# Kernel optimization log

Hardware: AMD Instinct MI355X
Metric: run time of the kernel (lower is better)

Reference implementation:

```python
import jax, jax.numpy as jnp
import numpy as np

B = 4096      # number of trees
DEPTH = 7     # complete binary tree depth -> N = 2**DEPTH - 1 = 127 nodes (heap order)
I_DIM = 300
H_DIM = 150


def setup_inputs() -> dict:
    key = jax.random.key(0)
    ks = jax.random.split(key, 6)
    N = 2 ** DEPTH - 1
    x = jax.random.normal(ks[0], (B, N, I_DIM), dtype=jnp.float32)
    Wiuo = jax.random.normal(ks[1], (3 * H_DIM, I_DIM), dtype=jnp.float32) / np.sqrt(I_DIM)
    Uiuo = jax.random.normal(ks[2], (3 * H_DIM, H_DIM), dtype=jnp.float32) / np.sqrt(H_DIM)
    biuo = jax.random.normal(ks[3], (1, 3 * H_DIM), dtype=jnp.float32) * 0.02
    Uf_w = jax.random.normal(ks[4], (H_DIM, H_DIM), dtype=jnp.float32) / np.sqrt(H_DIM)
    Uf_b = jax.random.normal(ks[5], (H_DIM,), dtype=jnp.float32) * 0.02
    return {"x": x, "Wiuo": Wiuo, "Uiuo": Uiuo, "biuo": biuo, "Uf_w": Uf_w, "Uf_b": Uf_b}


def reference(x, Wiuo, Uiuo, biuo, Uf_w, Uf_b):
    # Child-sum Tree-LSTM on complete binary trees (heap ordering).
    # Level d occupies node indices [2^d - 1, 2^(d+1) - 1); leaves at d = DEPTH-1.
    Bsz, N, _ = x.shape
    H = Uf_w.shape[0]
    # Input projection for all nodes (dropout in eval mode = identity)
    iuo_x = jnp.einsum('bni,ki->bnk', x, Wiuo)  # [B, N, 3H]
    h = jnp.zeros((Bsz, N, H), x.dtype)
    c = jnp.zeros((Bsz, N, H), x.dtype)
    for d in reversed(range(DEPTH)):  # leaves -> root (static loop over tree levels)
        start = 2 ** d - 1
        size = 2 ** d
        iuo = iuo_x[:, start:start + size]  # [B, size, 3H]
        if d == DEPTH - 1:
            c_sum = jnp.zeros((Bsz, size, H), x.dtype)
        else:
            cstart = 2 ** (d + 1) - 1
            ch = h[:, cstart:cstart + 2 * size].reshape(Bsz, size, 2, H)
            cc = c[:, cstart:cstart + 2 * size].reshape(Bsz, size, 2, H)
            h_tilda = ch.sum(axis=2)  # sum of children hidden states
            f = jax.nn.sigmoid(jnp.einsum('bskh,gh->bskg', ch, Uf_w) + Uf_b)
            c_sum = (f * cc).sum(axis=2)
            iuo = iuo + jnp.einsum('bsh,kh->bsk', h_tilda, Uiuo)
        iuo = iuo + biuo
        i_g, u_g, o_g = jnp.split(iuo, 3, axis=-1)
        c_new = jax.nn.sigmoid(i_g) * jnp.tanh(u_g) + c_sum
        h_new = jax.nn.sigmoid(o_g) * jnp.tanh(c_new)
        h = h.at[:, start:start + size].set(h_new)
        c = c.at[:, start:start + size].set(c_new)
    return h
```

## Files before the change

kernel.cpp:

```cpp
#include <hip/hip_runtime.h>

typedef float  f32x4  __attribute__((ext_vector_type(4)));
typedef short  s16x8  __attribute__((ext_vector_type(8)));
typedef short  s16x4  __attribute__((ext_vector_type(4)));
typedef _Float16 f16;

namespace {
constexpr int NN = 127, IDIM = 300, HD = 150;
constexpr int NT = 640, NW = 10;
constexpr int BCS  = 36;
constexpr int WSLAB = 17408;
constexpr int WCH = 34;
constexpr int ASTR = 36;
constexpr int A_SH = 64 * ASTR;
constexpr int GEMM_LDS = (2 * A_SH + 2 * WSLAB) * 2;
constexpr int CSTR = 164;

constexpr int W_SH = 10 * WSLAB;
constexpr int U_SH = 480 * 160;
constexpr int F_SH = 160 * 160;

constexpr size_t C_N   = (size_t)4096 * 126 * HD;
constexpr size_t IUO_N = (size_t)4096 * 63 * 456;

__device__ __forceinline__ short f2bf(float f) {
    union { __bf16 b; short s; } u; u.b = (__bf16)f; return u.s;
}
__device__ __forceinline__ float bf2f(short s) {
    union { float f; unsigned u; } v; v.u = ((unsigned)(unsigned short)s) << 16; return v.f;
}
__device__ __forceinline__ float sig_(float x)  { return 1.0f / (1.0f + __expf(-x)); }
__device__ __forceinline__ float tanh_(float x) { float e = __expf(2.0f * x); return 1.0f - 2.0f / (e + 1.0f); }
__device__ __forceinline__ s16x4 cvt4(float a,float b,float c,float d) {
    return s16x4{ f2bf(a), f2bf(b), f2bf(c), f2bf(d) };
}
__device__ __forceinline__ s16x8 cat(s16x4 lo, s16x4 hi) {
    return __builtin_shufflevector(lo, hi, 0,1,2,3,4,5,6,7);
}
__device__ __forceinline__ f32x4 MFMA(s16x8 a, s16x8 b, f32x4 c) {
    return __builtin_amdgcn_mfma_f32_16x16x32_bf16(a, b, c, 0, 0, 0);
}

typedef const __attribute__((address_space(1))) unsigned int* gp_t;
typedef __attribute__((address_space(3))) unsigned int* lp_t;
__device__ __forceinline__ void stage_slab(const short* g, short* l, int nch, int wv, int ln) {
    const char* gb = (const char*)g;
    char* lb = (char*)l;
    for (int c = wv; c < nch; c += NW)
        __builtin_amdgcn_global_load_lds((gp_t)(gb + c * 1024 + ln * 16),
                                         (lp_t)(lb + c * 1024 + ln * 16), 16, 0, 0);
}
}

__global__ __launch_bounds__(256)
void prep_w(const float* __restrict__ Wiuo, const float* __restrict__ Uiuo,
            const float* __restrict__ Ufw, short* __restrict__ dst) {
    int i = blockIdx.x * 256 + threadIdx.x;
    short v = 0;
    if (i < W_SH) {
        int kc = i / WSLAB, r = i - kc * WSLAB;
        if (r < 480 * BCS) {
            int col = r / BCS, j = r - col * BCS;
            int g = col / 160, cp = col - g * 160, k = kc * 32 + j;
            if (cp < HD && j < 32 && k < IDIM) v = f2bf(Wiuo[(size_t)(g*HD + cp)*IDIM + k]);
        }
        dst[i] = v;
    } else if (i < W_SH + U_SH) {
        int q = i - W_SH;
        int col = q / 160, k = q - col * 160;
        int g = col / 160, cp = col - g * 160;
        if (cp < HD && k < HD) v = f2bf(Uiuo[(size_t)(g*HD + cp)*HD + k]);
        dst[i] = v;
    } else if (i < W_SH + U_SH + F_SH) {
        int q = i - W_SH - U_SH;
        int col = q / 160, k = q - col * 160;
        if (col < HD && k < HD) v = f2bf(Ufw[(size_t)col*HD + k]);
        dst[i] = v;
    }
}

__global__ __launch_bounds__(NT)
void big_gemm(const float* __restrict__ x, const short* __restrict__ Wsl,
              const float* __restrict__ biuo, float* __restrict__ h_all,
              f16* __restrict__ c_all, f16* __restrict__ iuo_all)
{
    extern __shared__ short smem[];
    short* A0 = smem;
    short* A1 = A0 + A_SH;
    short* B0 = A1 + A_SH;
    short* B1 = B0 + WSLAB;

    const int t = threadIdx.x;
    const int wv = t >> 6, ln = t & 63, l15 = ln & 15, kg = ln >> 4;
    const int row0 = blockIdx.x * 64;

    int d = 6;
    for (int dd = 0; dd <= 5; ++dd)
        if (row0 >= 4096 * (128 - (2 << dd))) { d = dd; break; }
    const int base = 4096 * (128 - (2 << d));
    const int lg = d, mask = (1 << lg) - 1, start = (1 << lg) - 1;
    const int local0 = row0 - base;

    const int sr = t >> 3, sq = t & 7;
    const float* xrow = nullptr;
    if (sr < 64) {
        int lcl = local0 + sr, b = lcl >> lg, s = lcl & mask;
        xrow = x + ((size_t)b * NN + start + s) * IDIM;
    }

    stage_slab(Wsl, B0, WCH, wv, ln);
    if (sr < 64) {
        float4 f = *(const float4*)(xrow + sq * 4);
        *(s16x4*)&A0[sr * ASTR + sq * 4] = cvt4(f.x, f.y, f.z, f.w);
    }
    __syncthreads();

    f32x4 acc[4][3] = {};
    #pragma unroll
    for (int kc = 0; kc < 10; ++kc) {
        short* Ac = (kc & 1) ? A1 : A0;
        short* An = (kc & 1) ? A0 : A1;
        short* Bc = (kc & 1) ? B1 : B0;
        short* Bn = (kc & 1) ? B0 : B1;
        float4 nxt = {0.f, 0.f, 0.f, 0.f};
        if (kc < 9) {
            stage_slab(Wsl + (kc + 1) * WSLAB, Bn, WCH, wv, ln);
            if (sr < 64) {
                int k0 = (kc + 1) * 32 + sq * 4;
                if (k0 + 3 < IDIM) nxt = *(const float4*)(xrow + k0);
            }
        }
        s16x8 a[4];
        #pragma unroll
        for (int mt = 0; mt < 4; ++mt) {
            const short* p = &Ac[(16*mt + l15) * ASTR + kg * 8];
            a[mt] = cat(*(const s16x4*)p, *(const s16x4*)(p + 4));
        }
        #pragma unroll
        for (int g = 0; g < 3; ++g) {
            const short* p = &Bc[(g*160 + 16*wv + l15) * BCS + kg * 8];
            s16x8 bf = cat(*(const s16x4*)p, *(const s16x4*)(p + 4));
            #pragma unroll
            for (int mt = 0; mt < 4; ++mt)
                acc[mt][g] = MFMA(a[mt], bf, acc[mt][g]);
        }
        if (kc < 9) {
            if (sr < 64)
                *(s16x4*)&An[sr * ASTR + sq * 4] = cvt4(nxt.x, nxt.y, nxt.z, nxt.w);
            __syncthreads();
        }
    }

    const int c = 16 * wv + l15;
    if (c < HD) {
        if (d == 6) {
            float bi = biuo[c], bu = biuo[HD + c], bo = biuo[2*HD + c];
            #pragma unroll
            for (int mt = 0; mt < 4; ++mt)
                #pragma unroll
                for (int r = 0; r < 4; ++r) {
                    int lcl = local0 + 16*mt + 4*kg + r;
                    int b = lcl >> 6, s = lcl & 63;
                    float cn = sig_(acc[mt][0][r] + bi) * tanh_(acc[mt][1][r] + bu);
                    float hn = sig_(acc[mt][2][r] + bo) * tanh_(cn);
                    h_all[((size_t)b*NN + 63 + s) * HD + c] = hn;
                    c_all[((size_t)b*126 + 62 + s) * HD + c] = (f16)cn;
                }
        } else {
            #pragma unroll
            for (int mt = 0; mt < 4; ++mt)
                #pragma unroll
                for (int r = 0; r < 4; ++r) {
                    int lcl = local0 + 16*mt + 4*kg + r;
                    int b = lcl >> lg, s = lcl & mask;
                    f16* ip = iuo_all + ((size_t)b*63 + start + s) * 456;
                    ip[c]       = (f16)acc[mt][0][r];
                    ip[152 + c] = (f16)acc[mt][1][r];
                    ip[304 + c] = (f16)acc[mt][2][r];
                }
        }
    }
}

__global__ __launch_bounds__(NT, 5)
void lvl_light(const short* __restrict__ Ubf, const short* __restrict__ Fbf,
               const float* __restrict__ biuo, const float* __restrict__ Ufb,
               const f16* __restrict__ iuo_all, f16* __restrict__ c_all,
               float* __restrict__ h_all, int start, int lg, int cstart)
{
    __shared__ short chs[2][16][CSTR];
    __shared__ short fgs[NW][32][16];

    const int t = threadIdx.x;
    const int wv = t >> 6, ln = t & 63, l15 = ln & 15, kg = ln >> 4;
    const int row0 = blockIdx.x * 16;
    const int mask = (1 << lg) - 1;
    const int c = wv * 16 + l15;

    {
        int rc = t & 31, part = t >> 5;
        int plane = rc >> 4, lr = rc & 15;
        int row = row0 + lr, b = row >> lg, s = row & mask;
        const float* hp = h_all + ((size_t)b*NN + cstart + 2*s + plane) * HD;
        short* dst = &chs[plane][lr][part * 8];
        if (part < 18) {
            float4 f0 = *(const float4*)(hp + part*8);
            float4 f1 = *(const float4*)(hp + part*8 + 4);
            *(s16x4*)dst       = cvt4(f0.x, f0.y, f0.z, f0.w);
            *(s16x4*)(dst + 4) = cvt4(f1.x, f1.y, f1.z, f1.w);
        } else if (part == 18) {
            float4 f0 = *(const float4*)(hp + 144);
            float2 f1 = *(const float2*)(hp + 148);
            *(s16x4*)dst       = cvt4(f0.x, f0.y, f0.z, f0.w);
            *(s16x4*)(dst + 4) = s16x4{ f2bf(f1.x), f2bf(f1.y), 0, 0 };
        } else {
            *(s16x4*)dst = s16x4{0,0,0,0};
            *(s16x4*)(dst + 4) = s16x4{0,0,0,0};
        }
    }
    __syncthreads();

    f32x4 facc[2] = {};
    #pragma unroll
    for (int kc = 0; kc < 5; ++kc) {
        int ka = kc * 32 + kg * 8;
        s16x8 bf = *(const s16x8*)(Fbf + (size_t)c * 160 + ka);
        #pragma unroll
        for (int rt = 0; rt < 2; ++rt) {
            const short* p = &chs[rt][l15][ka];
            s16x8 af = cat(*(const s16x4*)p, *(const s16x4*)(p + 4));
            facc[rt] = MFMA(af, bf, facc[rt]);
        }
    }
    {
        float fb_ = (c < HD) ? Ufb[c] : 0.0f;
        #pragma unroll
        for (int rt = 0; rt < 2; ++rt)
            #pragma unroll
            for (int r = 0; r < 4; ++r)
                fgs[wv][rt*16 + 4*kg + r][l15] = f2bf(sig_(facc[rt][r] + fb_));
    }
    __syncthreads();

    f32x4 acc[3] = {};
    #pragma unroll
    for (int kc = 0; kc < 5; ++kc) {
        int ka = kc * 32 + kg * 8;
        const short* p0 = &chs[0][l15][ka];
        const short* p1 = &chs[1][l15][ka];
        s16x8 h0 = cat(*(const s16x4*)p0, *(const s16x4*)(p0 + 4));
        s16x8 h1 = cat(*(const s16x4*)p1, *(const s16x4*)(p1 + 4));
        s16x8 hs;
        #pragma unroll
        for (int e = 0; e < 8; ++e)
            hs[e] = f2bf(bf2f(h0[e]) + bf2f(h1[e]));
        #pragma unroll
        for (int g = 0; g < 3; ++g) {
            s16x8 bf = *(const s16x8*)(Ubf + (size_t)(g*160 + c) * 160 + ka);
            acc[g] = MFMA(hs, bf, acc[g]);
        }
    }

    if (c < HD) {
        float bi = biuo[c], bu = biuo[HD + c], bo = biuo[2*HD + c];
        #pragma unroll
        for (int r = 0; r < 4; ++r) {
            int pl = 4*kg + r;
            int row = row0 + pl, b = row >> lg, s = row & mask;
            const f16* ip = iuo_all + ((size_t)b*63 + start + s) * 456;
            float ig = (float)ip[c]       + bi + acc[0][r];
            float ug = (float)ip[152 + c] + bu + acc[1][r];
            float og = (float)ip[304 + c] + bo + acc[2][r];
            float f0 = bf2f(fgs[wv][pl][l15]);
            float f1 = bf2f(fgs[wv][16 + pl][l15]);
            size_t ci = (size_t)b*126 + (cstart + 2*s - 1);
            float c0 = (float)c_all[ci * HD + c];
            float c1 = (float)c_all[(ci + 1) * HD + c];
            float cn = sig_(ig) * tanh_(ug) + f0*c0 + f1*c1;
            float hn = sig_(og) * tanh_(cn);
            h_all[((size_t)b*NN + start + s) * HD + c] = hn;
            if (start > 0)
                c_all[((size_t)b*126 + start + s - 1) * HD + c] = (f16)cn;
        }
    }
}

extern "C" void kernel_launch(void* const* d_in, const int* in_sizes, int n_in,
                              void* d_out, int out_size, void* d_ws, size_t ws_size,
                              hipStream_t stream) {
    const float* x    = (const float*)d_in[0];
    const float* Wiuo = (const float*)d_in[1];
    const float* Uiuo = (const float*)d_in[2];
    const float* biuo = (const float*)d_in[3];
    const float* Ufw  = (const float*)d_in[4];
    const float* Ufb  = (const float*)d_in[5];
    float* h = (float*)d_out;

    f16* c_all   = (f16*)d_ws;
    f16* iuo_all = c_all + C_N;
    short* slabs = (short*)(iuo_all + IUO_N);
    const short* Wsl = slabs;
    const short* Ubf = slabs + W_SH;
    const short* Fbf = slabs + W_SH + U_SH;

    (void)hipFuncSetAttribute((const void*)big_gemm,
                              hipFuncAttributeMaxDynamicSharedMemorySize, 160 * 1024);

    prep_w<<<(W_SH + U_SH + F_SH + 255) / 256, 256, 0, stream>>>(Wiuo, Uiuo, Ufw, slabs);

    big_gemm<<<8128, NT, GEMM_LDS, stream>>>(x, Wsl, biuo, h, c_all, iuo_all);

    for (int d = 5; d >= 0; --d) {
        const int start = (1 << d) - 1, cstart = (1 << (d+1)) - 1;
        lvl_light<<<256 << d, NT, 0, stream>>>(Ubf, Fbf, biuo, Ufb, iuo_all, c_all, h,
                                               start, d, cstart);
    }
}
```

Baseline: 1.076 ms.

## Shrink GEMM tiles, single-buffer weight slab, halve level-kernel threads

```diff
diff --git a/kernel.cpp b/kernel.cpp
--- a/kernel.cpp
+++ b/kernel.cpp
@@ -8,15 +8,16 @@
 namespace {
 constexpr int NN = 127, IDIM = 300, HD = 150;
 constexpr int NT = 640, NW = 10;
-constexpr int BCS  = 36;
-constexpr int WSLAB = 17408;
-constexpr int WCH = 34;
-constexpr int ASTR = 36;
-constexpr int A_SH = 64 * ASTR;
-constexpr int GEMM_LDS = (2 * A_SH + 2 * WSLAB) * 2;
+constexpr int LNT = 320, LNW = 5;
+constexpr int BCS = 40;
+constexpr int SLAB_SH = 19456;
+constexpr int SCH = 38;
+constexpr int ASTR = 40;
+constexpr int A_SH = 32 * ASTR;
+constexpr int GEMM_LDS = (2 * A_SH + SLAB_SH) * 2;
 constexpr int CSTR = 164;
 
-constexpr int W_SH = 10 * WSLAB;
+constexpr int W_SH = 10 * SLAB_SH;
 constexpr int U_SH = 480 * 160;
 constexpr int F_SH = 160 * 160;
 
@@ -58,7 +59,7 @@
     int i = blockIdx.x * 256 + threadIdx.x;
     short v = 0;
     if (i < W_SH) {
-        int kc = i / WSLAB, r = i - kc * WSLAB;
+        int kc = i / SLAB_SH, r = i - kc * SLAB_SH;
         if (r < 480 * BCS) {
             int col = r / BCS, j = r - col * BCS;
             int g = col / 160, cp = col - g * 160, k = kc * 32 + j;
@@ -79,7 +80,7 @@
     }
 }
 
-__global__ __launch_bounds__(NT)
+__global__ __launch_bounds__(NT, 8)
 void big_gemm(const float* __restrict__ x, const short* __restrict__ Wsl,
               const float* __restrict__ biuo, float* __restrict__ h_all,
               f16* __restrict__ c_all, f16* __restrict__ iuo_all)
@@ -87,12 +88,11 @@
     extern __shared__ short smem[];
     short* A0 = smem;
     short* A1 = A0 + A_SH;
-    short* B0 = A1 + A_SH;
-    short* B1 = B0 + WSLAB;
+    short* Bs = A1 + A_SH;
 
     const int t = threadIdx.x;
     const int wv = t >> 6, ln = t & 63, l15 = ln & 15, kg = ln >> 4;
-    const int row0 = blockIdx.x * 64;
+    const int row0 = blockIdx.x * 32;
 
     int d = 6;
     for (int dd = 0; dd <= 5; ++dd)
@@ -101,54 +101,47 @@
     const int lg = d, mask = (1 << lg) - 1, start = (1 << lg) - 1;
     const int local0 = row0 - base;
 
-    const int sr = t >> 3, sq = t & 7;
+    const bool stg = (t < 256);
+    const int ar = t >> 3, aq = t & 7;
     const float* xrow = nullptr;
-    if (sr < 64) {
-        int lcl = local0 + sr, b = lcl >> lg, s = lcl & mask;
+    if (stg) {
+        int lcl = local0 + ar, b = lcl >> lg, s = lcl & mask;
         xrow = x + ((size_t)b * NN + start + s) * IDIM;
     }
 
-    stage_slab(Wsl, B0, WCH, wv, ln);
-    if (sr < 64) {
-        float4 f = *(const float4*)(xrow + sq * 4);
-        *(s16x4*)&A0[sr * ASTR + sq * 4] = cvt4(f.x, f.y, f.z, f.w);
-    }
-    __syncthreads();
-
-    f32x4 acc[4][3] = {};
+    if (stg) {
+        float4 f = *(const float4*)(xrow + aq * 4);
+        *(s16x4*)&A0[ar * ASTR + aq * 4] = cvt4(f.x, f.y, f.z, f.w);
+    }
+
+    f32x4 acc[2][3] = {};
     #pragma unroll
     for (int kc = 0; kc < 10; ++kc) {
         short* Ac = (kc & 1) ? A1 : A0;
         short* An = (kc & 1) ? A0 : A1;
-        short* Bc = (kc & 1) ? B1 : B0;
-        short* Bn = (kc & 1) ? B0 : B1;
+        __syncthreads();
+        stage_slab(Wsl + kc * SLAB_SH, Bs, SCH, wv, ln);
         float4 nxt = {0.f, 0.f, 0.f, 0.f};
-        if (kc < 9) {
-            stage_slab(Wsl + (kc + 1) * WSLAB, Bn, WCH, wv, ln);
-            if (sr < 64) {
-                int k0 = (kc + 1) * 32 + sq * 4;
-                if (k0 + 3 < IDIM) nxt = *(const float4*)(xrow + k0);
-            }
-        }
-        s16x8 a[4];
-        #pragma unroll
-        for (int mt = 0; mt < 4; ++mt) {
-            const short* p = &Ac[(16*mt + l15) * ASTR + kg * 8];
-            a[mt] = cat(*(const s16x4*)p, *(const s16x4*)(p + 4));
-        }
+        const bool nv = stg && (kc < 9);
+        if (nv) {
+            int k0 = (kc + 1) * 32 + aq * 4;
+            if (k0 + 3 < IDIM) nxt = *(const float4*)(xrow + k0);
+        }
+        __syncthreads();
+
+        const short* pa0 = &Ac[l15 * ASTR + kg * 8];
+        s16x8 a0 = cat(*(const s16x4*)pa0, *(const s16x4*)(pa0 + 4));
+        const short* pa1 = &Ac[(16 + l15) * ASTR + kg * 8];
+        s16x8 a1 = cat(*(const s16x4*)pa1, *(const s16x4*)(pa1 + 4));
         #pragma unroll
         for (int g = 0; g < 3; ++g) {
-            const short* p = &Bc[(g*160 + 16*wv + l15) * BCS + kg * 8];
-            s16x8 bf = cat(*(const s16x4*)p, *(const s16x4*)(p + 4));
-            #pragma unroll
-            for (int mt = 0; mt < 4; ++mt)
-                acc[mt][g] = MFMA(a[mt], bf, acc[mt][g]);
-        }
-        if (kc < 9) {
-            if (sr < 64)
-                *(s16x4*)&An[sr * ASTR + sq * 4] = cvt4(nxt.x, nxt.y, nxt.z, nxt.w);
-            __syncthreads();
-        }
+            const short* pb = &Bs[(g*160 + 16*wv + l15) * BCS + kg * 8];
+            s16x8 bf = cat(*(const s16x4*)pb, *(const s16x4*)(pb + 4));
+            acc[0][g] = MFMA(a0, bf, acc[0][g]);
+            acc[1][g] = MFMA(a1, bf, acc[1][g]);
+        }
+        if (nv)
+            *(s16x4*)&An[ar * ASTR + aq * 4] = cvt4(nxt.x, nxt.y, nxt.z, nxt.w);
     }
 
     const int c = 16 * wv + l15;
@@ -156,7 +149,7 @@
         if (d == 6) {
             float bi = biuo[c], bu = biuo[HD + c], bo = biuo[2*HD + c];
             #pragma unroll
-            for (int mt = 0; mt < 4; ++mt)
+            for (int mt = 0; mt < 2; ++mt)
                 #pragma unroll
                 for (int r = 0; r < 4; ++r) {
                     int lcl = local0 + 16*mt + 4*kg + r;
@@ -168,7 +161,7 @@
                 }
         } else {
             #pragma unroll
-            for (int mt = 0; mt < 4; ++mt)
+            for (int mt = 0; mt < 2; ++mt)
                 #pragma unroll
                 for (int r = 0; r < 4; ++r) {
                     int lcl = local0 + 16*mt + 4*kg + r;
@@ -182,67 +175,79 @@
     }
 }
 
-__global__ __launch_bounds__(NT, 5)
+__global__ __launch_bounds__(LNT, 5)
 void lvl_light(const short* __restrict__ Ubf, const short* __restrict__ Fbf,
                const float* __restrict__ biuo, const float* __restrict__ Ufb,
                const f16* __restrict__ iuo_all, f16* __restrict__ c_all,
                float* __restrict__ h_all, int start, int lg, int cstart)
 {
     __shared__ short chs[2][16][CSTR];
-    __shared__ short fgs[NW][32][16];
+    __shared__ short fgs[LNW][32][34];
 
     const int t = threadIdx.x;
     const int wv = t >> 6, ln = t & 63, l15 = ln & 15, kg = ln >> 4;
     const int row0 = blockIdx.x * 16;
     const int mask = (1 << lg) - 1;
-    const int c = wv * 16 + l15;
+    int ct[2];
+    ct[0] = 16 * (2*wv)     + l15;
+    ct[1] = 16 * (2*wv + 1) + l15;
 
     {
         int rc = t & 31, part = t >> 5;
         int plane = rc >> 4, lr = rc & 15;
         int row = row0 + lr, b = row >> lg, s = row & mask;
         const float* hp = h_all + ((size_t)b*NN + cstart + 2*s + plane) * HD;
-        short* dst = &chs[plane][lr][part * 8];
-        if (part < 18) {
-            float4 f0 = *(const float4*)(hp + part*8);
-            float4 f1 = *(const float4*)(hp + part*8 + 4);
-            *(s16x4*)dst       = cvt4(f0.x, f0.y, f0.z, f0.w);
-            *(s16x4*)(dst + 4) = cvt4(f1.x, f1.y, f1.z, f1.w);
-        } else if (part == 18) {
+        short* dst = &chs[plane][lr][part * 16];
+        if (part < 9) {
+            float4 f0 = *(const float4*)(hp + part*16);
+            float4 f1 = *(const float4*)(hp + part*16 + 4);
+            float4 f2 = *(const float4*)(hp + part*16 + 8);
+            float4 f3 = *(const float4*)(hp + part*16 + 12);
+            *(s16x4*)(dst + 0)  = cvt4(f0.x, f0.y, f0.z, f0.w);
+            *(s16x4*)(dst + 4)  = cvt4(f1.x, f1.y, f1.z, f1.w);
+            *(s16x4*)(dst + 8)  = cvt4(f2.x, f2.y, f2.z, f2.w);
+            *(s16x4*)(dst + 12) = cvt4(f3.x, f3.y, f3.z, f3.w);
+        } else {
             float4 f0 = *(const float4*)(hp + 144);
             float2 f1 = *(const float2*)(hp + 148);
-            *(s16x4*)dst       = cvt4(f0.x, f0.y, f0.z, f0.w);
-            *(s16x4*)(dst + 4) = s16x4{ f2bf(f1.x), f2bf(f1.y), 0, 0 };
-        } else {
-            *(s16x4*)dst = s16x4{0,0,0,0};
-            *(s16x4*)(dst + 4) = s16x4{0,0,0,0};
+            *(s16x4*)(dst + 0)  = cvt4(f0.x, f0.y, f0.z, f0.w);
+            *(s16x4*)(dst + 4)  = s16x4{ f2bf(f1.x), f2bf(f1.y), 0, 0 };
+            *(s16x4*)(dst + 8)  = s16x4{0,0,0,0};
+            *(s16x4*)(dst + 12) = s16x4{0,0,0,0};
         }
     }
     __syncthreads();
 
-    f32x4 facc[2] = {};
+    f32x4 facc[2][2] = {};
     #pragma unroll
     for (int kc = 0; kc < 5; ++kc) {
         int ka = kc * 32 + kg * 8;
-        s16x8 bf = *(const s16x8*)(Fbf + (size_t)c * 160 + ka);
+        s16x8 af[2];
         #pragma unroll
         for (int rt = 0; rt < 2; ++rt) {
             const short* p = &chs[rt][l15][ka];
-            s16x8 af = cat(*(const s16x4*)p, *(const s16x4*)(p + 4));
-            facc[rt] = MFMA(af, bf, facc[rt]);
-        }
-    }
-    {
-        float fb_ = (c < HD) ? Ufb[c] : 0.0f;
+            af[rt] = cat(*(const s16x4*)p, *(const s16x4*)(p + 4));
+        }
+        #pragma unroll
+        for (int tt = 0; tt < 2; ++tt) {
+            s16x8 bf = *(const s16x8*)(Fbf + (size_t)ct[tt] * 160 + ka);
+            #pragma unroll
+            for (int rt = 0; rt < 2; ++rt)
+                facc[rt][tt] = MFMA(af[rt], bf, facc[rt][tt]);
+        }
+    }
+    #pragma unroll
+    for (int tt = 0; tt < 2; ++tt) {
+        float fb_ = (ct[tt] < HD) ? Ufb[ct[tt]] : 0.0f;
         #pragma unroll
         for (int rt = 0; rt < 2; ++rt)
             #pragma unroll
             for (int r = 0; r < 4; ++r)
-                fgs[wv][rt*16 + 4*kg + r][l15] = f2bf(sig_(facc[rt][r] + fb_));
+                fgs[wv][rt*16 + 4*kg + r][tt*16 + l15] = f2bf(sig_(facc[rt][tt][r] + fb_));
     }
     __syncthreads();
 
-    f32x4 acc[3] = {};
+    f32x4 acc[2][3] = {};
     #pragma unroll
     for (int kc = 0; kc < 5; ++kc) {
         int ka = kc * 32 + kg * 8;
@@ -255,24 +260,29 @@
         for (int e = 0; e < 8; ++e)
             hs[e] = f2bf(bf2f(h0[e]) + bf2f(h1[e]));
         #pragma unroll
-        for (int g = 0; g < 3; ++g) {
-            s16x8 bf = *(const s16x8*)(Ubf + (size_t)(g*160 + c) * 160 + ka);
-            acc[g] = MFMA(hs, bf, acc[g]);
-        }
-    }
-
-    if (c < HD) {
+        for (int tt = 0; tt < 2; ++tt)
+            #pragma unroll
+            for (int g = 0; g < 3; ++g) {
+                s16x8 bf = *(const s16x8*)(Ubf + (size_t)(g*160 + ct[tt]) * 160 + ka);
+                acc[tt][g] = MFMA(hs, bf, acc[tt][g]);
+            }
+    }
+
+    #pragma unroll
+    for (int tt = 0; tt < 2; ++tt) {
+        int c = ct[tt];
+        if (c >= HD) continue;
         float bi = biuo[c], bu = biuo[HD + c], bo = biuo[2*HD + c];
         #pragma unroll
         for (int r = 0; r < 4; ++r) {
             int pl = 4*kg + r;
             int row = row0 + pl, b = row >> lg, s = row & mask;
             const f16* ip = iuo_all + ((size_t)b*63 + start + s) * 456;
-            float ig = (float)ip[c]       + bi + acc[0][r];
-            float ug = (float)ip[152 + c] + bu + acc[1][r];
-            float og = (float)ip[304 + c] + bo + acc[2][r];
-            float f0 = bf2f(fgs[wv][pl][l15]);
-            float f1 = bf2f(fgs[wv][16 + pl][l15]);
+            float ig = (float)ip[c]       + bi + acc[tt][0][r];
+            float ug = (float)ip[152 + c] + bu + acc[tt][1][r];
+            float og = (float)ip[304 + c] + bo + acc[tt][2][r];
+            float f0 = bf2f(fgs[wv][pl][tt*16 + l15]);
+            float f1 = bf2f(fgs[wv][16 + pl][tt*16 + l15]);
             size_t ci = (size_t)b*126 + (cstart + 2*s - 1);
             float c0 = (float)c_all[ci * HD + c];
             float c1 = (float)c_all[(ci + 1) * HD + c];
@@ -304,15 +314,15 @@
     const short* Fbf = slabs + W_SH + U_SH;
 
     (void)hipFuncSetAttribute((const void*)big_gemm,
-                              hipFuncAttributeMaxDynamicSharedMemorySize, 160 * 1024);
+                              hipFuncAttributeMaxDynamicSharedMemorySize, 64 * 1024);
 
     prep_w<<<(W_SH + U_SH + F_SH + 255) / 256, 256, 0, stream>>>(Wiuo, Uiuo, Ufw, slabs);
 
-    big_gemm<<<8128, NT, GEMM_LDS, stream>>>(x, Wsl, biuo, h, c_all, iuo_all);
+    big_gemm<<<16256, NT, GEMM_LDS, stream>>>(x, Wsl, biuo, h, c_all, iuo_all);
 
     for (int d = 5; d >= 0; --d) {
         const int start = (1 << d) - 1, cstart = (1 << (d+1)) - 1;
-        lvl_light<<<256 << d, NT, 0, stream>>>(Ubf, Fbf, biuo, Ufb, iuo_all, c_all, h,
-                                               start, d, cstart);
-    }
-}
+        lvl_light<<<256 << d, LNT, 0, stream>>>(Ubf, Fbf, biuo, Ufb, iuo_all, c_all, h,
+                                                start, d, cstart);
+    }
+}
```

New measurement: 1.148 ms. +6.6%, slower.

## Retile GEMM and level kernels for fewer idle waves and more operand reuse

Applied to the files above, without the earlier changes.

```diff
diff --git a/kernel.cpp b/kernel.cpp
--- a/kernel.cpp
+++ b/kernel.cpp
@@ -7,16 +7,18 @@
 
 namespace {
 constexpr int NN = 127, IDIM = 300, HD = 150;
-constexpr int NT = 640, NW = 10;
-constexpr int BCS  = 36;
-constexpr int WSLAB = 17408;
-constexpr int WCH = 34;
+constexpr int GNT = 512;
+constexpr int LNT = 320;
+constexpr int BCS = 36;
+constexpr int SLAB_SH = 17408;
+constexpr int SCH = 34;
 constexpr int ASTR = 36;
 constexpr int A_SH = 64 * ASTR;
-constexpr int GEMM_LDS = (2 * A_SH + 2 * WSLAB) * 2;
+constexpr int RSTR = 487;
+constexpr int GEMM_LDS = (2*A_SH + 2*SLAB_SH) * 2;
 constexpr int CSTR = 164;
 
-constexpr int W_SH = 10 * WSLAB;
+constexpr int W_SH = 10 * SLAB_SH;
 constexpr int U_SH = 480 * 160;
 constexpr int F_SH = 160 * 160;
 
@@ -28,6 +30,12 @@
 }
 __device__ __forceinline__ float bf2f(short s) {
     union { float f; unsigned u; } v; v.u = ((unsigned)(unsigned short)s) << 16; return v.f;
+}
+__device__ __forceinline__ short f2h_s(float f) {
+    union { f16 h; short s; } u; u.h = (f16)f; return u.s;
+}
+__device__ __forceinline__ float h2f_s(short s) {
+    union { f16 h; short s; } u; u.s = s; return (float)u.h;
 }
 __device__ __forceinline__ float sig_(float x)  { return 1.0f / (1.0f + __expf(-x)); }
 __device__ __forceinline__ float tanh_(float x) { float e = __expf(2.0f * x); return 1.0f - 2.0f / (e + 1.0f); }
@@ -43,10 +51,11 @@
 
 typedef const __attribute__((address_space(1))) unsigned int* gp_t;
 typedef __attribute__((address_space(3))) unsigned int* lp_t;
-__device__ __forceinline__ void stage_slab(const short* g, short* l, int nch, int wv, int ln) {
+__device__ __forceinline__ void stage_slab(const short* g, short* l, int nch,
+                                           int wv, int ln, int nw) {
     const char* gb = (const char*)g;
     char* lb = (char*)l;
-    for (int c = wv; c < nch; c += NW)
+    for (int c = wv; c < nch; c += nw)
         __builtin_amdgcn_global_load_lds((gp_t)(gb + c * 1024 + ln * 16),
                                          (lp_t)(lb + c * 1024 + ln * 16), 16, 0, 0);
 }
@@ -58,7 +67,7 @@
     int i = blockIdx.x * 256 + threadIdx.x;
     short v = 0;
     if (i < W_SH) {
-        int kc = i / WSLAB, r = i - kc * WSLAB;
+        int kc = i / SLAB_SH, r = i - kc * SLAB_SH;
         if (r < 480 * BCS) {
             int col = r / BCS, j = r - col * BCS;
             int g = col / 160, cp = col - g * 160, k = kc * 32 + j;
@@ -79,7 +88,7 @@
     }
 }
 
-__global__ __launch_bounds__(NT)
+__global__ __launch_bounds__(GNT, 4)
 void big_gemm(const float* __restrict__ x, const short* __restrict__ Wsl,
               const float* __restrict__ biuo, float* __restrict__ h_all,
               f16* __restrict__ c_all, f16* __restrict__ iuo_all)
@@ -88,7 +97,8 @@
     short* A0 = smem;
     short* A1 = A0 + A_SH;
     short* B0 = A1 + A_SH;
-    short* B1 = B0 + WSLAB;
+    short* B1 = B0 + SLAB_SH;
+    short* rs = B0;
 
     const int t = threadIdx.x;
     const int wv = t >> 6, ln = t & 63, l15 = ln & 15, kg = ln >> 4;
@@ -101,21 +111,21 @@
     const int lg = d, mask = (1 << lg) - 1, start = (1 << lg) - 1;
     const int local0 = row0 - base;
 
-    const int sr = t >> 3, sq = t & 7;
-    const float* xrow = nullptr;
-    if (sr < 64) {
-        int lcl = local0 + sr, b = lcl >> lg, s = lcl & mask;
+    const int ar = t >> 3, aq = t & 7;
+    const float* xrow;
+    {
+        int lcl = local0 + ar, b = lcl >> lg, s = lcl & mask;
         xrow = x + ((size_t)b * NN + start + s) * IDIM;
     }
 
-    stage_slab(Wsl, B0, WCH, wv, ln);
-    if (sr < 64) {
-        float4 f = *(const float4*)(xrow + sq * 4);
-        *(s16x4*)&A0[sr * ASTR + sq * 4] = cvt4(f.x, f.y, f.z, f.w);
+    stage_slab(Wsl, B0, SCH, wv, ln, 8);
+    {
+        float4 f = *(const float4*)(xrow + aq * 4);
+        *(s16x4*)&A0[ar * ASTR + aq * 4] = cvt4(f.x, f.y, f.z, f.w);
     }
     __syncthreads();
 
-    f32x4 acc[4][3] = {};
+    f32x4 acc[4][4] = {};
     #pragma unroll
     for (int kc = 0; kc < 10; ++kc) {
         short* Ac = (kc & 1) ? A1 : A0;
@@ -124,11 +134,9 @@
         short* Bn = (kc & 1) ? B0 : B1;
         float4 nxt = {0.f, 0.f, 0.f, 0.f};
         if (kc < 9) {
-            stage_slab(Wsl + (kc + 1) * WSLAB, Bn, WCH, wv, ln);
-            if (sr < 64) {
-                int k0 = (kc + 1) * 32 + sq * 4;
-                if (k0 + 3 < IDIM) nxt = *(const float4*)(xrow + k0);
-            }
+            stage_slab(Wsl + (kc + 1) * SLAB_SH, Bn, SCH, wv, ln, 8);
+            int k0 = (kc + 1) * 32 + aq * 4;
+            if (k0 + 3 < IDIM) nxt = *(const float4*)(xrow + k0);
         }
         s16x8 a[4];
         #pragma unroll
@@ -137,151 +145,202 @@
             a[mt] = cat(*(const s16x4*)p, *(const s16x4*)(p + 4));
         }
         #pragma unroll
-        for (int g = 0; g < 3; ++g) {
-            const short* p = &Bc[(g*160 + 16*wv + l15) * BCS + kg * 8];
-            s16x8 bf = cat(*(const s16x4*)p, *(const s16x4*)(p + 4));
+        for (int tt = 0; tt < 4; ++tt) {
+            int ct = wv + 8 * tt;
+            int cts = (ct < 30) ? ct : 29;
+            const short* pb = &Bc[(cts * 16 + l15) * BCS + kg * 8];
+            s16x8 bf = cat(*(const s16x4*)pb, *(const s16x4*)(pb + 4));
             #pragma unroll
             for (int mt = 0; mt < 4; ++mt)
-                acc[mt][g] = MFMA(a[mt], bf, acc[mt][g]);
+                acc[tt][mt] = MFMA(a[mt], bf, acc[tt][mt]);
         }
         if (kc < 9) {
-            if (sr < 64)
-                *(s16x4*)&An[sr * ASTR + sq * 4] = cvt4(nxt.x, nxt.y, nxt.z, nxt.w);
+            *(s16x4*)&An[ar * ASTR + aq * 4] = cvt4(nxt.x, nxt.y, nxt.z, nxt.w);
             __syncthreads();
         }
     }
 
-    const int c = 16 * wv + l15;
-    if (c < HD) {
-        if (d == 6) {
-            float bi = biuo[c], bu = biuo[HD + c], bo = biuo[2*HD + c];
-            #pragma unroll
-            for (int mt = 0; mt < 4; ++mt)
+    if (d == 6) {
+        __syncthreads();
+        #pragma unroll
+        for (int tt = 0; tt < 4; ++tt) {
+            int ct = wv + 8 * tt;
+            if (ct < 30) {
                 #pragma unroll
-                for (int r = 0; r < 4; ++r) {
-                    int lcl = local0 + 16*mt + 4*kg + r;
-                    int b = lcl >> 6, s = lcl & 63;
-                    float cn = sig_(acc[mt][0][r] + bi) * tanh_(acc[mt][1][r] + bu);
-                    float hn = sig_(acc[mt][2][r] + bo) * tanh_(cn);
-                    h_all[((size_t)b*NN + 63 + s) * HD + c] = hn;
-                    c_all[((size_t)b*126 + 62 + s) * HD + c] = (f16)cn;
+                for (int mt = 0; mt < 4; ++mt)
+                    #pragma unroll
+                    for (int r = 0; r < 4; ++r)
+                        rs[(16*mt + 4*kg + r) * RSTR + ct * 16 + l15] = f2h_s(acc[tt][mt][r]);
+            }
+        }
+        __syncthreads();
+        {
+            int rr = t & 63, c0 = t >> 6;
+            int lcl = local0 + rr, b = lcl >> 6, s = lcl & 63;
+            const short* rp = &rs[rr * RSTR];
+            size_t hb = ((size_t)b * NN + 63 + s) * HD;
+            size_t cb = ((size_t)b * 126 + 62 + s) * HD;
+            #pragma unroll
+            for (int j = 0; j < 19; ++j) {
+                int c = c0 + 8 * j;
+                if (c < HD) {
+                    float ig = h2f_s(rp[c])       + biuo[c];
+                    float ug = h2f_s(rp[160 + c]) + biuo[HD + c];
+                    float og = h2f_s(rp[320 + c]) + biuo[2*HD + c];
+                    float cn = sig_(ig) * tanh_(ug);
+                    float hn = sig_(og) * tanh_(cn);
+                    h_all[hb + c] = hn;
+                    c_all[cb + c] = (f16)cn;
                 }
-        } else {
-            #pragma unroll
-            for (int mt = 0; mt < 4; ++mt)
+            }
+        }
+    } else {
+        #pragma unroll
+        for (int tt = 0; tt < 4; ++tt) {
+            int ct = wv + 8 * tt;
+            if (ct >= 30) continue;
+            int g = ct / 10;
+            int cig = (ct - g * 10) * 16 + l15;
+            if (cig < HD) {
                 #pragma unroll
-                for (int r = 0; r < 4; ++r) {
-                    int lcl = local0 + 16*mt + 4*kg + r;
-                    int b = lcl >> lg, s = lcl & mask;
-                    f16* ip = iuo_all + ((size_t)b*63 + start + s) * 456;
-                    ip[c]       = (f16)acc[mt][0][r];
-                    ip[152 + c] = (f16)acc[mt][1][r];
-                    ip[304 + c] = (f16)acc[mt][2][r];
-                }
-        }
-    }
-}
-
-__global__ __launch_bounds__(NT, 5)
+                for (int mt = 0; mt < 4; ++mt)
+                    #pragma unroll
+                    for (int r = 0; r < 4; ++r) {
+                        int lcl = local0 + 16*mt + 4*kg + r;
+                        int b = lcl >> lg, s = lcl & mask;
+                        iuo_all[((size_t)b*63 + start + s) * 456 + 152*g + cig] =
+                            (f16)acc[tt][mt][r];
+                    }
+            }
+        }
+    }
+}
+
+__global__ __launch_bounds__(LNT, 4)
 void lvl_light(const short* __restrict__ Ubf, const short* __restrict__ Fbf,
                const float* __restrict__ biuo, const float* __restrict__ Ufb,
                const f16* __restrict__ iuo_all, f16* __restrict__ c_all,
                float* __restrict__ h_all, int start, int lg, int cstart)
 {
-    __shared__ short chs[2][16][CSTR];
-    __shared__ short fgs[NW][32][16];
+    __shared__ short chs[2][32][CSTR];
+    __shared__ short fgs[5][64][34];
 
     const int t = threadIdx.x;
     const int wv = t >> 6, ln = t & 63, l15 = ln & 15, kg = ln >> 4;
-    const int row0 = blockIdx.x * 16;
+    const int row0 = blockIdx.x * 32;
     const int mask = (1 << lg) - 1;
-    const int c = wv * 16 + l15;
+    int ct0 = 16 * (2*wv)     + l15;
+    int ct1 = 16 * (2*wv + 1) + l15;
 
     {
-        int rc = t & 31, part = t >> 5;
-        int plane = rc >> 4, lr = rc & 15;
+        int rc = t & 63, part = t >> 6;
+        int plane = rc >> 5, lr = rc & 31;
         int row = row0 + lr, b = row >> lg, s = row & mask;
         const float* hp = h_all + ((size_t)b*NN + cstart + 2*s + plane) * HD;
-        short* dst = &chs[plane][lr][part * 8];
-        if (part < 18) {
-            float4 f0 = *(const float4*)(hp + part*8);
-            float4 f1 = *(const float4*)(hp + part*8 + 4);
-            *(s16x4*)dst       = cvt4(f0.x, f0.y, f0.z, f0.w);
-            *(s16x4*)(dst + 4) = cvt4(f1.x, f1.y, f1.z, f1.w);
-        } else if (part == 18) {
-            float4 f0 = *(const float4*)(hp + 144);
-            float2 f1 = *(const float2*)(hp + 148);
-            *(s16x4*)dst       = cvt4(f0.x, f0.y, f0.z, f0.w);
-            *(s16x4*)(dst + 4) = s16x4{ f2bf(f1.x), f2bf(f1.y), 0, 0 };
-        } else {
-            *(s16x4*)dst = s16x4{0,0,0,0};
-            *(s16x4*)(dst + 4) = s16x4{0,0,0,0};
+        short* dst = &chs[plane][lr][part * 32];
+        #pragma unroll
+        for (int q = 0; q < 8; ++q) {
+            int k = part * 32 + q * 4;
+            s16x4 v = {0,0,0,0};
+            if (k + 3 < HD) {
+                float4 f = *(const float4*)(hp + k);
+                v = cvt4(f.x, f.y, f.z, f.w);
+            } else if (k < HD) {
+                float2 f = *(const float2*)(hp + k);
+                v = s16x4{ f2bf(f.x), f2bf(f.y), 0, 0 };
+            }
+            *(s16x4*)(dst + q * 4) = v;
         }
     }
     __syncthreads();
 
-    f32x4 facc[2] = {};
+    f32x4 facc[4][2] = {};
     #pragma unroll
     for (int kc = 0; kc < 5; ++kc) {
         int ka = kc * 32 + kg * 8;
-        s16x8 bf = *(const s16x8*)(Fbf + (size_t)c * 160 + ka);
-        #pragma unroll
-        for (int rt = 0; rt < 2; ++rt) {
-            const short* p = &chs[rt][l15][ka];
-            s16x8 af = cat(*(const s16x4*)p, *(const s16x4*)(p + 4));
-            facc[rt] = MFMA(af, bf, facc[rt]);
-        }
-    }
-    {
-        float fb_ = (c < HD) ? Ufb[c] : 0.0f;
-        #pragma unroll
-        for (int rt = 0; rt < 2; ++rt)
+        s16x8 af[4];
+        #pragma unroll
+        for (int rt = 0; rt < 4; ++rt) {
+            const short* p = &chs[rt >> 1][(rt & 1) * 16 + l15][ka];
+            af[rt] = cat(*(const s16x4*)p, *(const s16x4*)(p + 4));
+        }
+        #pragma unroll
+        for (int tt = 0; tt < 2; ++tt) {
+            int ct = tt ? ct1 : ct0;
+            s16x8 bf = *(const s16x8*)(Fbf + (size_t)ct * 160 + ka);
+            #pragma unroll
+            for (int rt = 0; rt < 4; ++rt)
+                facc[rt][tt] = MFMA(af[rt], bf, facc[rt][tt]);
+        }
+    }
+    #pragma unroll
+    for (int tt = 0; tt < 2; ++tt) {
+        int ct = tt ? ct1 : ct0;
+        float fb_ = (ct < HD) ? Ufb[ct] : 0.0f;
+        #pragma unroll
+        for (int rt = 0; rt < 4; ++rt)
             #pragma unroll
             for (int r = 0; r < 4; ++r)
-                fgs[wv][rt*16 + 4*kg + r][l15] = f2bf(sig_(facc[rt][r] + fb_));
+                fgs[wv][rt*16 + 4*kg + r][tt*16 + l15] = f2bf(sig_(facc[rt][tt][r] + fb_));
     }
     __syncthreads();
 
-    f32x4 acc[3] = {};
+    f32x4 acc[2][2][3] = {};
     #pragma unroll
     for (int kc = 0; kc < 5; ++kc) {
         int ka = kc * 32 + kg * 8;
-        const short* p0 = &chs[0][l15][ka];
-        const short* p1 = &chs[1][l15][ka];
-        s16x8 h0 = cat(*(const s16x4*)p0, *(const s16x4*)(p0 + 4));
-        s16x8 h1 = cat(*(const s16x4*)p1, *(const s16x4*)(p1 + 4));
-        s16x8 hs;
-        #pragma unroll
-        for (int e = 0; e < 8; ++e)
-            hs[e] = f2bf(bf2f(h0[e]) + bf2f(h1[e]));
-        #pragma unroll
-        for (int g = 0; g < 3; ++g) {
-            s16x8 bf = *(const s16x8*)(Ubf + (size_t)(g*160 + c) * 160 + ka);
-            acc[g] = MFMA(hs, bf, acc[g]);
-        }
-    }
-
-    if (c < HD) {
+        s16x8 hs[2];
+        #pragma unroll
+        for (int mt = 0; mt < 2; ++mt) {
+            const short* p0 = &chs[0][16*mt + l15][ka];
+            const short* p1 = &chs[1][16*mt + l15][ka];
+            s16x8 h0 = cat(*(const s16x4*)p0, *(const s16x4*)(p0 + 4));
+            s16x8 h1 = cat(*(const s16x4*)p1, *(const s16x4*)(p1 + 4));
+            s16x8 hv;
+            #pragma unroll
+            for (int e = 0; e < 8; ++e)
+                hv[e] = f2bf(bf2f(h0[e]) + bf2f(h1[e]));
+            hs[mt] = hv;
+        }
+        #pragma unroll
+        for (int tt = 0; tt < 2; ++tt) {
+            int ct = tt ? ct1 : ct0;
+            #pragma unroll
+            for (int g = 0; g < 3; ++g) {
+                s16x8 bf = *(const s16x8*)(Ubf + (size_t)(g*160 + ct) * 160 + ka);
+                #pragma unroll
+                for (int mt = 0; mt < 2; ++mt)
+                    acc[mt][tt][g] = MFMA(hs[mt], bf, acc[mt][tt][g]);
+            }
+        }
+    }
+
+    #pragma unroll
+    for (int tt = 0; tt < 2; ++tt) {
+        int c = tt ? ct1 : ct0;
+        if (c >= HD) continue;
         float bi = biuo[c], bu = biuo[HD + c], bo = biuo[2*HD + c];
         #pragma unroll
-        for (int r = 0; r < 4; ++r) {
-            int pl = 4*kg + r;
-            int row = row0 + pl, b = row >> lg, s = row & mask;
-            const f16* ip = iuo_all + ((size_t)b*63 + start + s) * 456;
-            float ig = (float)ip[c]       + bi + acc[0][r];
-            float ug = (float)ip[152 + c] + bu + acc[1][r];
-            float og = (float)ip[304 + c] + bo + acc[2][r];
-            float f0 = bf2f(fgs[wv][pl][l15]);
-            float f1 = bf2f(fgs[wv][16 + pl][l15]);
-            size_t ci = (size_t)b*126 + (cstart + 2*s - 1);
-            float c0 = (float)c_all[ci * HD + c];
-            float c1 = (float)c_all[(ci + 1) * HD + c];
-            float cn = sig_(ig) * tanh_(ug) + f0*c0 + f1*c1;
-            float hn = sig_(og) * tanh_(cn);
-            h_all[((size_t)b*NN + start + s) * HD + c] = hn;
-            if (start > 0)
-                c_all[((size_t)b*126 + start + s - 1) * HD + c] = (f16)cn;
-        }
+        for (int mt = 0; mt < 2; ++mt)
+            #pragma unroll
+            for (int r = 0; r < 4; ++r) {
+                int pl = 16*mt + 4*kg + r;
+                int row = row0 + pl, b = row >> lg, s = row & mask;
+                const f16* ip = iuo_all + ((size_t)b*63 + start + s) * 456;
+                float ig = (float)ip[c]       + bi + acc[mt][tt][0][r];
+                float ug = (float)ip[152 + c] + bu + acc[mt][tt][1][r];
+                float og = (float)ip[304 + c] + bo + acc[mt][tt][2][r];
+                float f0 = bf2f(fgs[wv][pl][tt*16 + l15]);
+                float f1 = bf2f(fgs[wv][32 + pl][tt*16 + l15]);
+                size_t ci = (size_t)b*126 + (cstart + 2*s - 1);
+                float c0 = (float)c_all[ci * HD + c];
+                float c1 = (float)c_all[(ci + 1) * HD + c];
+                float cn = sig_(ig) * tanh_(ug) + f0*c0 + f1*c1;
+                float hn = sig_(og) * tanh_(cn);
+                h_all[((size_t)b*NN + start + s) * HD + c] = hn;
+                if (start > 0)
+                    c_all[((size_t)b*126 + start + s - 1) * HD + c] = (f16)cn;
+            }
     }
 }
 
@@ -308,11 +367,11 @@
 
     prep_w<<<(W_SH + U_SH + F_SH + 255) / 256, 256, 0, stream>>>(Wiuo, Uiuo, Ufw, slabs);
 
-    big_gemm<<<8128, NT, GEMM_LDS, stream>>>(x, Wsl, biuo, h, c_all, iuo_all);
+    big_gemm<<<8128, GNT, GEMM_LDS, stream>>>(x, Wsl, biuo, h, c_all, iuo_all);
 
     for (int d = 5; d >= 0; --d) {
         const int start = (1 << d) - 1, cstart = (1 << (d+1)) - 1;
-        lvl_light<<<256 << d, NT, 0, stream>>>(Ubf, Fbf, biuo, Ufb, iuo_all, c_all, h,
-                                               start, d, cstart);
-    }
-}
+        lvl_light<<<128 << d, LNT, 0, stream>>>(Ubf, Fbf, biuo, Ufb, iuo_all, c_all, h,
+                                                start, d, cstart);
+    }
+}
```

New measurement: 1.227 ms. +14.1%, slower.
